# Kernel optimization log

Hardware: AMD Instinct MI355X
Metric: run time of the kernel (lower is better)

Reference implementation:

```python
import jax, jax.numpy as jnp
from jax import lax
import numpy as np

B, L, OBS_DIM, ACT_DIM = 4, 1024, 60, 2
D_MODEL, N_LAYERS, D_STATE, D_CONV, EXPAND = 256, 4, 16, 4, 2
D_INNER = EXPAND * D_MODEL
DT_RANK = (D_MODEL + 15) // 16  # mamba_ssm default: ceil(d_model/16)


def setup_inputs() -> dict:
    key = jax.random.key(0)
    ks = jax.random.split(key, 12)
    rn = lambda k, s, sc: jax.random.normal(k, s, jnp.float32) * sc
    return {
        "obs_seq": jax.random.normal(ks[0], (B, L, OBS_DIM), jnp.float32),
        "input_proj_w": rn(ks[1], (D_MODEL, OBS_DIM), OBS_DIM ** -0.5),
        "input_proj_b": jnp.zeros((D_MODEL,), jnp.float32),
        "norm_w": jnp.ones((N_LAYERS, D_MODEL), jnp.float32),
        "norm_b": jnp.zeros((N_LAYERS, D_MODEL), jnp.float32),
        "in_proj_w": rn(ks[2], (N_LAYERS, 2 * D_INNER, D_MODEL), D_MODEL ** -0.5),
        "conv_w": rn(ks[3], (N_LAYERS, D_INNER, D_CONV), D_CONV ** -0.5),
        "conv_b": jnp.zeros((N_LAYERS, D_INNER), jnp.float32),
        "x_proj_w": rn(ks[4], (N_LAYERS, DT_RANK + 2 * D_STATE, D_INNER), D_INNER ** -0.5),
        "dt_proj_w": rn(ks[5], (N_LAYERS, D_INNER, DT_RANK), DT_RANK ** -0.5),
        "dt_proj_b": jnp.full((N_LAYERS, D_INNER), float(np.log(np.expm1(0.01))), jnp.float32),
        "A_log": jnp.log(jnp.broadcast_to(jnp.arange(1, D_STATE + 1, dtype=jnp.float32), (N_LAYERS, D_INNER, D_STATE))),
        "D_skip": jnp.ones((N_LAYERS, D_INNER), jnp.float32),
        "out_proj_w": rn(ks[6], (N_LAYERS, D_MODEL, D_INNER), D_INNER ** -0.5),
        "policy_mean_w": rn(ks[7], (ACT_DIM, D_MODEL), 0.01 * D_MODEL ** -0.5),
        "policy_mean_b": jnp.zeros((ACT_DIM,), jnp.float32),
        "policy_log_std": jnp.zeros((ACT_DIM,), jnp.float32),
        "value_w": rn(ks[8], (1, D_MODEL), D_MODEL ** -0.5),
        "value_b": jnp.zeros((1,), jnp.float32),
    }


def _silu(x):
    return x * jax.nn.sigmoid(x)


def _layer_norm(x, w, b):
    m = jnp.mean(x, -1, keepdims=True)
    v = jnp.mean(jnp.square(x - m), -1, keepdims=True)
    return (x - m) * lax.rsqrt(v + 1e-5) * w + b


def _mamba(x, in_w, cw, cb, xw, dtw, dtb, a_log, d_skip, ow):
    # x: (B, L, d_model)
    xz = jnp.einsum('bld,ed->ble', x, in_w)            # (B, L, 2*d_inner)
    xi, z = xz[..., :D_INNER], xz[..., D_INNER:]
    # depthwise causal conv, width D_CONV
    xp = jnp.pad(xi, ((0, 0), (D_CONV - 1, 0), (0, 0)))
    conv = sum(xp[:, k:k + L, :] * cw[:, k] for k in range(D_CONV)) + cb
    xi = _silu(conv)
    dbc = jnp.einsum('bld,ed->ble', xi, xw)            # (B, L, dt_rank + 2*d_state)
    dt = jax.nn.softplus(jnp.einsum('blr,dr->bld', dbc[..., :DT_RANK], dtw) + dtb)
    Bm = dbc[..., DT_RANK:DT_RANK + D_STATE]           # (B, L, N)
    Cm = dbc[..., DT_RANK + D_STATE:]                  # (B, L, N)
    A = -jnp.exp(a_log)                                # (d_inner, N)
    dA = jnp.exp(dt[..., None] * A)                    # (B, L, d_inner, N)
    dBx = (dt * xi)[..., None] * Bm[:, :, None, :]     # (B, L, d_inner, N)

    def comb(c1, c2):
        a1, b1 = c1
        a2, b2 = c2
        return a2 * a1, a2 * b1 + b2

    _, h = lax.associative_scan(comb, (dA, dBx), axis=1)  # h_t = dA_t*h_{t-1} + dBx_t
    y = jnp.einsum('bldn,bln->bld', h, Cm) + d_skip * xi
    return jnp.einsum('bld,ed->ble', y * _silu(z), ow)


def _forward(obs_seq, input_proj_w, input_proj_b, norm_w, norm_b, in_proj_w, conv_w,
             conv_b, x_proj_w, dt_proj_w, dt_proj_b, A_log, D_skip, out_proj_w,
             policy_mean_w, policy_mean_b, policy_log_std, value_w, value_b):
    x = _silu(jnp.einsum('blo,do->bld', obs_seq, input_proj_w) + input_proj_b)
    for i in range(N_LAYERS):  # pre-norm residual Mamba blocks
        x = x + _mamba(_layer_norm(x, norm_w[i], norm_b[i]), in_proj_w[i], conv_w[i],
                       conv_b[i], x_proj_w[i], dt_proj_w[i], dt_proj_b[i], A_log[i],
                       D_skip[i], out_proj_w[i])
    mu = jnp.einsum('bld,ad->bla', x, policy_mean_w) + policy_mean_b
    std = jnp.broadcast_to(jnp.exp(policy_log_std), mu.shape)
    value = jnp.einsum('bld,od->blo', x, value_w) + value_b
    return mu, std, value


def reference(obs_seq, input_proj_w, input_proj_b, norm_w, norm_b, in_proj_w, conv_w,
              conv_b, x_proj_w, dt_proj_w, dt_proj_b, A_log, D_skip, out_proj_w,
              policy_mean_w, policy_mean_b, policy_log_std, value_w, value_b):
    return _forward(obs_seq, input_proj_w, input_proj_b, norm_w, norm_b, in_proj_w,
                    conv_w, conv_b, x_proj_w, dt_proj_w, dt_proj_b, A_log, D_skip,
                    out_proj_w, policy_mean_w, policy_mean_b, policy_log_std,
                    value_w, value_b)
```

## Files before the change

### kernel.cpp

```cpp
#include <hip/hip_runtime.h>
#include <hip/hip_bf16.h>

#define Bsz 4
#define Lseq 1024
#define OBS 60
#define DM 256
#define DI 512
#define DTR 16
#define DST 16
#define NTOK (Bsz*Lseq)
#define NCH 64
#define CH  16

typedef _Float16 half8 __attribute__((ext_vector_type(8)));
typedef float floatx4 __attribute__((ext_vector_type(4)));

__device__ __forceinline__ float silu_f(float v) {
    return v * (1.f / (1.f + __expf(-v)));
}
__device__ __forceinline__ float softplus_f(float v) {
    return fmaxf(v, 0.f) + log1pf(__expf(-fabsf(v)));
}

__device__ __forceinline__ void compute_dA(float dtv, const float* An,
                                           bool structured, float* dA) {
    if (structured) {
        float p1 = __expf(-dtv);
        float p2 = p1*p1, p4 = p2*p2, p8 = p4*p4;
        dA[0]=p1;      dA[1]=p2;      dA[2]=p2*p1;    dA[3]=p4;
        dA[4]=p4*p1;   dA[5]=p4*p2;   dA[6]=p4*dA[2]; dA[7]=p8;
        dA[8]=p8*p1;   dA[9]=p8*p2;   dA[10]=p8*dA[2];dA[11]=p8*p4;
        dA[12]=p8*dA[4];dA[13]=p8*dA[5];dA[14]=p8*dA[6];dA[15]=p8*p8;
    } else {
        #pragma unroll
        for (int n = 0; n < 16; ++n) dA[n] = __expf(dtv*An[n]);
    }
}

#define NIN_W  (4*1024*256)
#define NX_W   (4*64*512)
#define NOUT_W (4*256*512)
#define NCWT   (4*4*512)
#define NW_TOT (NIN_W + NX_W + NOUT_W + NCWT)
#define NWB    ((NW_TOT + 255)/256)
__global__ __launch_bounds__(256) void prep_kernel(
    const float* __restrict__ inw, const float* __restrict__ xw,
    const float* __restrict__ ow, const float* __restrict__ cw,
    _Float16* __restrict__ wh_in, _Float16* __restrict__ wh_x,
    _Float16* __restrict__ wh_out, _Float16* __restrict__ cwT,
    const float* __restrict__ obs, const float* __restrict__ ipw,
    const float* __restrict__ ipb, const float* __restrict__ nw,
    const float* __restrict__ nb, float* __restrict__ x,
    _Float16* __restrict__ xn_h) {
    __shared__ float so[OBS];
    __shared__ float ps[4];
    __shared__ float mean_s, rstd_s;
    int tid = threadIdx.x;
    if (blockIdx.x < NWB) {
        int idx = blockIdx.x*256 + tid;
        if (idx < NIN_W) {
            wh_in[idx] = (_Float16)inw[idx];
        } else if (idx < NIN_W + NX_W) {
            int r = idx - NIN_W;
            int layer = r >> 15;
            int rem = r & 32767;
            int n = rem >> 9, k = rem & 511;
            wh_x[r] = (_Float16)((n < 48) ? xw[((size_t)layer*48 + n)*512 + k] : 0.f);
        } else if (idx < NIN_W + NX_W + NOUT_W) {
            int r = idx - NIN_W - NX_W;
            wh_out[r] = (_Float16)ow[r];
        } else if (idx < NW_TOT) {
            int r = idx - NIN_W - NX_W - NOUT_W;
            int layer = r >> 11;
            int rem = r & 2047;
            int k = rem >> 9, d = rem & 511;
            cwT[r] = (_Float16)cw[layer*2048 + d*4 + k];
        }
        return;
    }
    int t = blockIdx.x - NWB;
    if (tid < OBS) so[tid] = obs[t*OBS + tid];
    __syncthreads();
    float acc = ipb[tid];
    const float* wr = ipw + tid*OBS;
    #pragma unroll
    for (int k = 0; k < OBS; ++k) acc += so[k]*wr[k];
    float v = silu_f(acc);
    x[t*DM + tid] = v;
    float s = v;
    #pragma unroll
    for (int off = 32; off; off >>= 1) s += __shfl_down(s, off);
    int wid = tid >> 6, lane = tid & 63;
    if (lane == 0) ps[wid] = s;
    __syncthreads();
    if (tid == 0) mean_s = (ps[0]+ps[1]+ps[2]+ps[3]) * (1.f/DM);
    __syncthreads();
    float m = mean_s;
    float d = v - m;
    float sq = d*d;
    #pragma unroll
    for (int off = 32; off; off >>= 1) sq += __shfl_down(sq, off);
    if (lane == 0) ps[wid] = sq;
    __syncthreads();
    if (tid == 0) rstd_s = rsqrtf((ps[0]+ps[1]+ps[2]+ps[3])*(1.f/DM) + 1e-5f);
    __syncthreads();
    xn_h[t*DM + tid] = (_Float16)(d * rstd_s * nw[tid] + nb[tid]);
}

template<int BM, int BN, int WM, int WN, int EPI>
__global__ __launch_bounds__(256) void hgemm_nt(
    const _Float16* __restrict__ A, const _Float16* __restrict__ W,
    void* __restrict__ Cout, const float* __restrict__ resid,
    int M, int N, int K, int ldc,
    const float* __restrict__ e0, const float* __restrict__ e1,
    const float* __restrict__ e2, const float* __restrict__ e3,
    const float* __restrict__ e4,
    float* __restrict__ xout, _Float16* __restrict__ xnh) {
    constexpr int MFR = BM/(WM*16);
    constexpr int NFR = BN/(WN*16);
    __shared__ _Float16 As[BM*64];
    __shared__ _Float16 Bs[BN*64];
    int tid = threadIdx.x;
    int r0 = blockIdx.y*BM, c0 = blockIdx.x*BN;
    int w = tid >> 6, lane = tid & 63;
    int wr = w / WN, wc = w % WN;
    floatx4 acc[MFR][NFR];
    #pragma unroll
    for (int i = 0; i < MFR; ++i)
        #pragma unroll
        for (int j = 0; j < NFR; ++j)
            acc[i][j] = (floatx4)0.f;

    for (int k0 = 0; k0 < K; k0 += 64) {
        #pragma unroll
        for (int c = 0; c < BM/32; ++c) {
            int q = tid + 256*c;
            int row = q >> 3, cc = (q & 7)*8;
            half8 v = *(const half8*)&A[(size_t)(r0 + row)*K + k0 + cc];
            *(half8*)&As[row*64 + (cc ^ ((row & 7) << 3))] = v;
        }
        #pragma unroll
        for (int c = 0; c < BN/32; ++c) {
            int q = tid + 256*c;
            int row = q >> 3, cc = (q & 7)*8;
            half8 v = *(const half8*)&W[(size_t)(c0 + row)*K + k0 + cc];
            *(half8*)&Bs[row*64 + (cc ^ ((row & 7) << 3))] = v;
        }
        __syncthreads();
        #pragma unroll
        for (int kc = 0; kc < 2; ++kc) {
            half8 a[MFR], b[NFR];
            int col = kc*32 + (lane >> 4)*8;
            #pragma unroll
            for (int i = 0; i < MFR; ++i) {
                int row = wr*(BM/WM) + i*16 + (lane & 15);
                a[i] = *(const half8*)&As[row*64 + (col ^ ((row & 7) << 3))];
            }
            #pragma unroll
            for (int j = 0; j < NFR; ++j) {
                int row = wc*(BN/WN) + j*16 + (lane & 15);
                b[j] = *(const half8*)&Bs[row*64 + (col ^ ((row & 7) << 3))];
            }
            #pragma unroll
            for (int i = 0; i < MFR; ++i)
                #pragma unroll
                for (int j = 0; j < NFR; ++j)
                    acc[i][j] = __builtin_amdgcn_mfma_f32_16x16x32_f16(a[i], b[j], acc[i][j], 0, 0, 0);
        }
        __syncthreads();
    }
    if constexpr (EPI == 1) {
        _Float16* C = (_Float16*)Cout;
        #pragma unroll
        for (int i = 0; i < MFR; ++i) {
            int m0 = r0 + wr*(BM/WM) + i*16 + (lane >> 4)*4;
            #pragma unroll
            for (int j = 0; j < NFR; ++j) {
                int col = c0 + wc*(BN/WN) + j*16 + (lane & 15);
                #pragma unroll
                for (int t = 0; t < 4; ++t)
                    C[(size_t)(m0 + t)*ldc + col] = (_Float16)acc[i][j][t];
            }
        }
    } else if constexpr (EPI == 2 || EPI == 3) {
        int g = lane >> 4, ln16 = lane & 15;
        #pragma unroll
        for (int t = 0; t < 4; ++t) {
            int row = r0 + wr*16 + g*4 + t;
            #pragma unroll
            for (int j = 0; j < NFR; ++j)
                acc[0][j][t] += resid[(size_t)row*DM + j*16 + ln16];
        }
        if constexpr (EPI == 2) {
            #pragma unroll
            for (int t = 0; t < 4; ++t) {
                int row = r0 + wr*16 + g*4 + t;
                float s = 0.f, sq = 0.f;
                #pragma unroll
                for (int j = 0; j < NFR; ++j) {
                    float v = acc[0][j][t];
                    xout[(size_t)row*DM + j*16 + ln16] = v;
                    s += v; sq += v*v;
                }
                #pragma unroll
                for (int msk = 1; msk < 16; msk <<= 1) {
                    s += __shfl_xor(s, msk);
                    sq += __shfl_xor(sq, msk);
                }
                float mean = s * (1.f/DM);
                float rstd = rsqrtf(sq*(1.f/DM) - mean*mean + 1e-5f);
                #pragma unroll
                for (int j = 0; j < NFR; ++j) {
                    int col = j*16 + ln16;
                    float v = acc[0][j][t];
                    xnh[(size_t)row*DM + col] =
                        (_Float16)((v - mean)*rstd*e0[col] + e1[col]);
                }
            }
        } else {
            float* out = xout;
            #pragma unroll
            for (int t = 0; t < 4; ++t) {
                int row = r0 + wr*16 + g*4 + t;
                float m0 = 0.f, m1 = 0.f, vv = 0.f;
                #pragma unroll
                for (int j = 0; j < NFR; ++j) {
                    int col = j*16 + ln16;
                    float v = acc[0][j][t];
                    m0 += v*e0[col]; m1 += v*e0[DM + col]; vv += v*e3[col];
                }
                #pragma unroll
                for (int msk = 1; msk < 16; msk <<= 1) {
                    m0 += __shfl_xor(m0, msk);
                    m1 += __shfl_xor(m1, msk);
                    vv += __shfl_xor(vv, msk);
                }
                if (ln16 == 0) {
                    out[row*2 + 0] = m0 + e1[0];
                    out[row*2 + 1] = m1 + e1[1];
                    out[2*NTOK + row*2 + 0] = __expf(e2[0]);
                    out[2*NTOK + row*2 + 1] = __expf(e2[1]);
                    out[4*NTOK + row] = vv + e4[0];
                }
            }
        }
    }
}

__global__ __launch_bounds__(256) void xproj_conv_gemm(
    const _Float16* __restrict__ xz_h, const _Float16* __restrict__ Wx,
    const _Float16* __restrict__ cwT, const float* __restrict__ cb,
    float* __restrict__ dbc) {
    __shared__ _Float16 As[32*64];
    __shared__ _Float16 Bs[64*64];
    int tid = threadIdx.x;
    int r0 = blockIdx.x*32;
    int w = tid >> 6, lane = tid & 63;
    int wr = w >> 1, wc = w & 1;
    floatx4 acc[2];
    acc[0] = (floatx4)0.f; acc[1] = (floatx4)0.f;
    for (int k0 = 0; k0 < 512; k0 += 64) {
        {
            int row = tid >> 3, e8 = tid & 7;
            int d = k0 + e8*8;
            int t = r0 + row, l = t & (Lseq-1);
            half8 zero8 = (half8)((_Float16)0.f);
            half8 v0 = (l >= 3) ? *(const half8*)&xz_h[(size_t)(t-3)*1024 + d] : zero8;
            half8 v1 = (l >= 2) ? *(const half8*)&xz_h[(size_t)(t-2)*1024 + d] : zero8;
            half8 v2 = (l >= 1) ? *(const half8*)&xz_h[(size_t)(t-1)*1024 + d] : zero8;
            half8 v3 = *(const half8*)&xz_h[(size_t)t*1024 + d];
            half8 c0 = *(const half8*)&cwT[0*512 + d];
            half8 c1 = *(const half8*)&cwT[1*512 + d];
            half8 c2 = *(const half8*)&cwT[2*512 + d];
            half8 c3 = *(const half8*)&cwT[3*512 + d];
            half8 o;
            #pragma unroll
            for (int e = 0; e < 8; ++e) {
                float a = cb[d + e];
                a += (float)v0[e]*(float)c0[e];
                a += (float)v1[e]*(float)c1[e];
                a += (float)v2[e]*(float)c2[e];
                a += (float)v3[e]*(float)c3[e];
                o[e] = (_Float16)silu_f(a);
            }
            *(half8*)&As[row*64 + ((e8*8) ^ ((row & 7) << 3))] = o;
        }
        #pragma unroll
        for (int c = 0; c < 2; ++c) {
            int q = tid + 256*c;
            int row = q >> 3, cc = (q & 7)*8;
            half8 vv = *(const half8*)&Wx[(size_t)row*512 + k0 + cc];
            *(half8*)&Bs[row*64 + (cc ^ ((row & 7) << 3))] = vv;
        }
        __syncthreads();
        #pragma unroll
        for (int kc = 0; kc < 2; ++kc) {
            int col = kc*32 + (lane >> 4)*8;
            int arow = wr*16 + (lane & 15);
            half8 a = *(const half8*)&As[arow*64 + (col ^ ((arow & 7) << 3))];
            #pragma unroll
            for (int j = 0; j < 2; ++j) {
                int brow = wc*32 + j*16 + (lane & 15);
                half8 b = *(const half8*)&Bs[brow*64 + (col ^ ((brow & 7) << 3))];
                acc[j] = __builtin_amdgcn_mfma_f32_16x16x32_f16(a, b, acc[j], 0, 0, 0);
            }
        }
        __syncthreads();
    }
    int m0 = r0 + wr*16 + (lane >> 4)*4;
    #pragma unroll
    for (int j = 0; j < 2; ++j) {
        int col = wc*32 + j*16 + (lane & 15);
        if (col < 48) {
            #pragma unroll
            for (int t = 0; t < 4; ++t)
                dbc[(size_t)(m0 + t)*48 + col] = acc[j][t];
        }
    }
}

__global__ __launch_bounds__(256) void scan_phaseA(
    const _Float16* __restrict__ xz_h, const float* __restrict__ dbc,
    const float* __restrict__ dtw, const float* __restrict__ dtb,
    const float* __restrict__ a_log, const float* __restrict__ cw,
    const float* __restrict__ cb,
    _Float16* __restrict__ xi_h,
    _Float16* __restrict__ Ap, _Float16* __restrict__ He) {
    __shared__ float sdbc[CH*48];
    int blk = blockIdx.x;
    int b = blk >> 7; int rem = blk & 127; int c = rem >> 1; int half = rem & 1;
    int d = half*256 + threadIdx.x;
    const float* src = dbc + ((size_t)(b*Lseq + c*CH))*48;
    for (int q = threadIdx.x; q < CH*48; q += 256) sdbc[q] = src[q];
    float wreg[16];
    #pragma unroll
    for (int r = 0; r < DTR; ++r) wreg[r] = dtw[d*DTR + r];
    float bias = dtb[d];
    float4 cwv = *(const float4*)&cw[d*4];
    float cbv = cb[d];
    float An[16];
    bool structured = true;
    #pragma unroll
    for (int n = 0; n < 16; ++n) {
        An[n] = -__expf(a_log[d*16 + n]);
        structured = structured && (fabsf(An[n] + (float)(n+1)) < 1e-4f*(n+1));
    }
    int l0 = c*CH; int t0 = b*Lseq + l0;
    float w0 = 0.f, w1 = 0.f, w2 = 0.f;
    if (l0 >= 3) {
        w0 = (float)xz_h[(size_t)(t0-3)*1024 + d];
        w1 = (float)xz_h[(size_t)(t0-2)*1024 + d];
        w2 = (float)xz_h[(size_t)(t0-1)*1024 + d];
    }
    __syncthreads();
    float h[16] = {};
    float ap[16];
    #pragma unroll
    for (int n = 0; n < 16; ++n) ap[n] = 1.f;
    for (int s = 0; s < CH; ++s) {
        float cur = (float)xz_h[(size_t)(t0+s)*1024 + d];
        float conv = cbv + cwv.x*w0 + cwv.y*w1 + cwv.z*w2 + cwv.w*cur;
        w0 = w1; w1 = w2; w2 = cur;
        float xiv = silu_f(conv);
        float dl = bias;
        #pragma unroll
        for (int r = 0; r < DTR; ++r) dl += sdbc[s*48 + r]*wreg[r];
        float dtv = softplus_f(dl);
        xi_h[(size_t)(t0+s)*DI + d] = (_Float16)xiv;
        float u = dtv*xiv;
        float dA[16];
        compute_dA(dtv, An, structured, dA);
        #pragma unroll
        for (int n = 0; n < 16; ++n) {
            h[n] = dA[n]*h[n] + u*sdbc[s*48 + DTR + n];
            ap[n] *= dA[n];
        }
    }
    size_t base = ((size_t)(b*NCH + c)*16)*DI + d;
    #pragma unroll
    for (int n = 0; n < 16; ++n) {
        Ap[base + n*DI] = (_Float16)ap[n];
        He[base + n*DI] = (_Float16)h[n];
    }
}

__global__ __launch_bounds__(256) void scan_phaseB(
    const _Float16* __restrict__ Ap, const _Float16* __restrict__ He,
    _Float16* __restrict__ h0) {
    int g = blockIdx.x*blockDim.x + threadIdx.x;
    int b = g >> 13; int n = (g >> 9) & 15; int d = g & 511;
    float run = 0.f;
    for (int c = 0; c < NCH; ++c) {
        size_t idx = ((size_t)(b*NCH + c)*16 + n)*DI + d;
        float a = (float)Ap[idx], e = (float)He[idx];
        h0[idx] = (_Float16)run;
        run = a*run + e;
    }
}

__global__ __launch_bounds__(256) void scan_phaseC(
    const _Float16* __restrict__ xi_h, const float* __restrict__ dbc,
    const float* __restrict__ dtw, const float* __restrict__ dtb,
    const float* __restrict__ a_log, const float* __restrict__ dskip,
    const _Float16* __restrict__ xz_h, const _Float16* __restrict__ h0,
    _Float16* __restrict__ yg_h) {
    __shared__ float sdbc[CH*48];
    int blk = blockIdx.x;
    int b = blk >> 7; int rem = blk & 127; int c = rem >> 1; int half = rem & 1;
    int d = half*256 + threadIdx.x;
    const float* src = dbc + ((size_t)(b*Lseq + c*CH))*48;
    for (int q = threadIdx.x; q < CH*48; q += 256) sdbc[q] = src[q];
    float wreg[16];
    #pragma unroll
    for (int r = 0; r < DTR; ++r) wreg[r] = dtw[d*DTR + r];
    float bias = dtb[d];
    float An[16];
    bool structured = true;
    #pragma unroll
    for (int n = 0; n < 16; ++n) {
        An[n] = -__expf(a_log[d*16 + n]);
        structured = structured && (fabsf(An[n] + (float)(n+1)) < 1e-4f*(n+1));
    }
    __syncthreads();
    int t0 = b*Lseq + c*CH;
    float h[16];
    size_t base = ((size_t)(b*NCH + c)*16)*DI + d;
    #pragma unroll
    for (int n = 0; n < 16; ++n) h[n] = (float)h0[base + n*DI];
    float ds = dskip[d];
    for (int s = 0; s < CH; ++s) {
        size_t ti = (size_t)(t0+s)*DI + d;
        float xiv = (float)xi_h[ti];
        float dl = bias;
        #pragma unroll
        for (int r = 0; r < DTR; ++r) dl += sdbc[s*48 + r]*wreg[r];
        float dtv = softplus_f(dl);
        float u = dtv*xiv;
        float dA[16];
        compute_dA(dtv, An, structured, dA);
        float y = ds*xiv;
        #pragma unroll
        for (int n = 0; n < 16; ++n) {
            h[n] = dA[n]*h[n] + u*sdbc[s*48 + DTR + n];
            y += h[n]*sdbc[s*48 + DTR + DST + n];
        }
        float zv = (float)xz_h[(size_t)(t0+s)*1024 + DI + d];
        yg_h[ti] = (_Float16)(y * silu_f(zv));
    }
}

extern "C" void kernel_launch(void* const* d_in, const int* in_sizes, int n_in,
                              void* d_out, int out_size, void* d_ws, size_t ws_size,
                              hipStream_t stream) {
    const float* obs = (const float*)d_in[0];
    const float* ipw = (const float*)d_in[1];
    const float* ipb = (const float*)d_in[2];
    const float* nw  = (const float*)d_in[3];
    const float* nb  = (const float*)d_in[4];
    const float* inw = (const float*)d_in[5];
    const float* cw  = (const float*)d_in[6];
    const float* cb  = (const float*)d_in[7];
    const float* xw  = (const float*)d_in[8];
    const float* dtw = (const float*)d_in[9];
    const float* dtb = (const float*)d_in[10];
    const float* alog= (const float*)d_in[11];
    const float* dsk = (const float*)d_in[12];
    const float* ow  = (const float*)d_in[13];
    const float* pw  = (const float*)d_in[14];
    const float* pb  = (const float*)d_in[15];
    const float* ls  = (const float*)d_in[16];
    const float* vw  = (const float*)d_in[17];
    const float* vb  = (const float*)d_in[18];
    float* out = (float*)d_out;

    float* ws = (float*)d_ws;
    float* x   = ws;
    float* dbc = x   + 1048576;
    _Float16* f16b  = (_Float16*)(dbc + 196608);
    _Float16* xz_h  = f16b;
    _Float16* xn_h  = xz_h  + 4194304;
    _Float16* xi_h  = xn_h  + 1048576;
    _Float16* yg_h  = xi_h  + 2097152;
    _Float16* Ap_h  = yg_h  + 2097152;
    _Float16* He_h  = Ap_h  + 2097152;
    _Float16* h0_h  = Ap_h;
    _Float16* wh_in = He_h  + 2097152;
    _Float16* wh_x  = wh_in + 1048576;
    _Float16* wh_out= wh_x  + 131072;
    _Float16* cwT_h = wh_out+ 524288;

    prep_kernel<<<NWB + NTOK, 256, 0, stream>>>(
        inw, xw, ow, cw, wh_in, wh_x, wh_out, cwT_h,
        obs, ipw, ipb, nw, nb, x, xn_h);

    for (int i = 0; i < 4; ++i) {
        {
            dim3 g(1024/64, NTOK/128);
            hgemm_nt<128,64,2,2,1><<<g, 256, 0, stream>>>(
                xn_h, wh_in + (size_t)i*1024*256, xz_h, nullptr, NTOK, 1024, 256, 1024,
                nullptr, nullptr, nullptr, nullptr, nullptr, nullptr, nullptr);
        }
        xproj_conv_gemm<<<NTOK/32, 256, 0, stream>>>(
            xz_h, wh_x + (size_t)i*64*512, cwT_h + i*2048, cb + i*DI, dbc);
        scan_phaseA<<<Bsz*NCH*2, 256, 0, stream>>>(
            xz_h, dbc, dtw + (size_t)i*DI*DTR, dtb + i*DI,
            alog + (size_t)i*DI*DST, cw + (size_t)i*DI*4, cb + i*DI,
            xi_h, Ap_h, He_h);
        scan_phaseB<<<128, 256, 0, stream>>>(Ap_h, He_h, h0_h);
        scan_phaseC<<<Bsz*NCH*2, 256, 0, stream>>>(
            xi_h, dbc, dtw + (size_t)i*DI*DTR, dtb + i*DI,
            alog + (size_t)i*DI*DST, dsk + i*DI, xz_h, h0_h, yg_h);
        {
            dim3 g(1, NTOK/64);
            if (i < 3) {
                hgemm_nt<64,256,4,1,2><<<g, 256, 0, stream>>>(
                    yg_h, wh_out + (size_t)i*256*512, nullptr, x, NTOK, 256, 512, 256,
                    nw + (i+1)*DM, nb + (i+1)*DM, nullptr, nullptr, nullptr, x, xn_h);
            } else {
                hgemm_nt<64,256,4,1,3><<<g, 256, 0, stream>>>(
                    yg_h, wh_out + (size_t)i*256*512, nullptr, x, NTOK, 256, 512, 256,
                    pw, pb, ls, vw, vb, out, nullptr);
            }
        }
    }
}
```

Measured before the change: 346.0 us.

## Fold dt_proj into x_proj weights and precompute dt via one fused GEMM

Precomputes the product of dt_proj and the dt rows of x_proj in the prep kernel, so a single GEMM (576 columns) produces the softplus'd dt per channel plus the B/C projections. The causal conv and SiLU move into a separate elementwise kernel that writes xi once. The scan kernels then read precomputed dt and xi from memory instead of recomputing the 16-term dt dot product and the conv per step, and they prefetch per-chunk inputs into registers. The cost is a much larger GEMM (512 extra output columns), an extra kernel launch, and an extra fp16 dt buffer written and read in every layer.

```diff
diff --git a/kernel.cpp b/kernel.cpp
--- a/kernel.cpp
+++ b/kernel.cpp
@@ -38,47 +38,68 @@
 }
 
 #define NIN_W  (4*1024*256)
-#define NX_W   (4*64*512)
 #define NOUT_W (4*256*512)
-#define NCWT   (4*4*512)
-#define NW_TOT (NIN_W + NX_W + NOUT_W + NCWT)
-#define NWB    ((NW_TOT + 255)/256)
+#define NS0    (NIN_W + NOUT_W)
+#define NB_S0  (NS0/256)
+#define NB_S1  (4*64*512/256)
+#define NB_S2  32
 __global__ __launch_bounds__(256) void prep_kernel(
-    const float* __restrict__ inw, const float* __restrict__ xw,
-    const float* __restrict__ ow, const float* __restrict__ cw,
-    _Float16* __restrict__ wh_in, _Float16* __restrict__ wh_x,
-    _Float16* __restrict__ wh_out, _Float16* __restrict__ cwT,
+    const float* __restrict__ inw, const float* __restrict__ ow,
+    const float* __restrict__ xw, const float* __restrict__ dtw,
+    _Float16* __restrict__ wh_in, _Float16* __restrict__ wh_out,
+    _Float16* __restrict__ Wbig,
     const float* __restrict__ obs, const float* __restrict__ ipw,
     const float* __restrict__ ipb, const float* __restrict__ nw,
     const float* __restrict__ nb, float* __restrict__ x,
     _Float16* __restrict__ xn_h) {
-    __shared__ float so[OBS];
+    __shared__ float swxT[512][16];
     __shared__ float ps[4];
     __shared__ float mean_s, rstd_s;
     int tid = threadIdx.x;
-    if (blockIdx.x < NWB) {
+    if (blockIdx.x < NB_S0) {
         int idx = blockIdx.x*256 + tid;
-        if (idx < NIN_W) {
-            wh_in[idx] = (_Float16)inw[idx];
-        } else if (idx < NIN_W + NX_W) {
-            int r = idx - NIN_W;
-            int layer = r >> 15;
-            int rem = r & 32767;
-            int n = rem >> 9, k = rem & 511;
-            wh_x[r] = (_Float16)((n < 48) ? xw[((size_t)layer*48 + n)*512 + k] : 0.f);
-        } else if (idx < NIN_W + NX_W + NOUT_W) {
-            int r = idx - NIN_W - NX_W;
-            wh_out[r] = (_Float16)ow[r];
-        } else if (idx < NW_TOT) {
-            int r = idx - NIN_W - NX_W - NOUT_W;
-            int layer = r >> 11;
-            int rem = r & 2047;
-            int k = rem >> 9, d = rem & 511;
-            cwT[r] = (_Float16)cw[layer*2048 + d*4 + k];
-        }
+        if (idx < NIN_W) wh_in[idx] = (_Float16)inw[idx];
+        else wh_out[idx - NIN_W] = (_Float16)ow[idx - NIN_W];
         return;
     }
-    int t = blockIdx.x - NWB;
+    if (blockIdx.x < NB_S0 + NB_S1) {
+        int idx = (blockIdx.x - NB_S0)*256 + tid;
+        int L = idx >> 15;
+        int rem = idx & 32767;
+        int j = rem >> 9, k = rem & 511;
+        float v = (j < 32) ? xw[(size_t)L*48*512 + (size_t)(16 + j)*512 + k] : 0.f;
+        Wbig[(size_t)L*576*512 + (size_t)(512 + j)*512 + k] = (_Float16)v;
+        return;
+    }
+    if (blockIdx.x < NB_S0 + NB_S1 + NB_S2) {
+        int q2 = blockIdx.x - NB_S0 - NB_S1;
+        int L = q2 >> 3, E = q2 & 7;
+        const float* xwL = xw + (size_t)L*48*512;
+        #pragma unroll
+        for (int i = 0; i < 32; ++i) {
+            int q = tid + 256*i;
+            int r = q >> 9, k = q & 511;
+            swxT[k][r] = xwL[(size_t)r*512 + k];
+        }
+        __syncthreads();
+        int e = E*64 + (tid >> 2), kq = tid & 3;
+        float dwr[16];
+        const float* dtwp = dtw + ((size_t)L*512 + e)*16;
+        #pragma unroll
+        for (int r = 0; r < 16; ++r) dwr[r] = dtwp[r];
+        _Float16* wb = Wbig + (size_t)L*576*512 + (size_t)e*512;
+        for (int kk = 0; kk < 128; ++kk) {
+            int k = kq*128 + kk;
+            const float* sp = &swxT[k][0];
+            float acc = 0.f;
+            #pragma unroll
+            for (int r = 0; r < 16; ++r) acc += dwr[r]*sp[r];
+            wb[k] = (_Float16)acc;
+        }
+        return;
+    }
+    int t = blockIdx.x - NB_S0 - NB_S1 - NB_S2;
+    __shared__ float so[OBS];
     if (tid < OBS) so[tid] = obs[t*OBS + tid];
     __syncthreads();
     float acc = ipb[tid];
@@ -96,15 +117,15 @@
     if (tid == 0) mean_s = (ps[0]+ps[1]+ps[2]+ps[3]) * (1.f/DM);
     __syncthreads();
     float m = mean_s;
-    float d = v - m;
-    float sq = d*d;
+    float dd = v - m;
+    float sq = dd*dd;
     #pragma unroll
     for (int off = 32; off; off >>= 1) sq += __shfl_down(sq, off);
     if (lane == 0) ps[wid] = sq;
     __syncthreads();
     if (tid == 0) rstd_s = rsqrtf((ps[0]+ps[1]+ps[2]+ps[3])*(1.f/DM) + 1e-5f);
     __syncthreads();
-    xn_h[t*DM + tid] = (_Float16)(d * rstd_s * nw[tid] + nb[tid]);
+    xn_h[t*DM + tid] = (_Float16)(dd * rstd_s * nw[tid] + nb[tid]);
 }
 
 template<int BM, int BN, int WM, int WN, int EPI>
@@ -247,50 +268,46 @@
     }
 }
 
-__global__ __launch_bounds__(256) void xproj_conv_gemm(
-    const _Float16* __restrict__ xz_h, const _Float16* __restrict__ Wx,
-    const _Float16* __restrict__ cwT, const float* __restrict__ cb,
-    float* __restrict__ dbc) {
+__global__ __launch_bounds__(256) void conv_silu_kernel(
+    const _Float16* __restrict__ xz_h, const float* __restrict__ cw,
+    const float* __restrict__ cb, _Float16* __restrict__ xi_h) {
+    int idx = blockIdx.x*blockDim.x + threadIdx.x;
+    if (idx >= NTOK*DI) return;
+    int d = idx & (DI-1); int t = idx >> 9;
+    int l = t & (Lseq-1);
+    float acc = cb[d];
+    #pragma unroll
+    for (int k = 0; k < 4; ++k) {
+        int ls = l - 3 + k;
+        if (ls >= 0) acc += (float)xz_h[(size_t)(t-3+k)*1024 + d] * cw[d*4 + k];
+    }
+    xi_h[idx] = (_Float16)silu_f(acc);
+}
+
+__global__ __launch_bounds__(256) void big_gemm(
+    const _Float16* __restrict__ xi_h, const _Float16* __restrict__ Wb,
+    const float* __restrict__ dtb, _Float16* __restrict__ dt_h,
+    float* __restrict__ dbc32) {
     __shared__ _Float16 As[32*64];
     __shared__ _Float16 Bs[64*64];
     int tid = threadIdx.x;
-    int r0 = blockIdx.x*32;
+    int r0 = blockIdx.y*32, c0 = blockIdx.x*64;
     int w = tid >> 6, lane = tid & 63;
     int wr = w >> 1, wc = w & 1;
     floatx4 acc[2];
     acc[0] = (floatx4)0.f; acc[1] = (floatx4)0.f;
     for (int k0 = 0; k0 < 512; k0 += 64) {
         {
-            int row = tid >> 3, e8 = tid & 7;
-            int d = k0 + e8*8;
-            int t = r0 + row, l = t & (Lseq-1);
-            half8 zero8 = (half8)((_Float16)0.f);
-            half8 v0 = (l >= 3) ? *(const half8*)&xz_h[(size_t)(t-3)*1024 + d] : zero8;
-            half8 v1 = (l >= 2) ? *(const half8*)&xz_h[(size_t)(t-2)*1024 + d] : zero8;
-            half8 v2 = (l >= 1) ? *(const half8*)&xz_h[(size_t)(t-1)*1024 + d] : zero8;
-            half8 v3 = *(const half8*)&xz_h[(size_t)t*1024 + d];
-            half8 c0 = *(const half8*)&cwT[0*512 + d];
-            half8 c1 = *(const half8*)&cwT[1*512 + d];
-            half8 c2 = *(const half8*)&cwT[2*512 + d];
-            half8 c3 = *(const half8*)&cwT[3*512 + d];
-            half8 o;
-            #pragma unroll
-            for (int e = 0; e < 8; ++e) {
-                float a = cb[d + e];
-                a += (float)v0[e]*(float)c0[e];
-                a += (float)v1[e]*(float)c1[e];
-                a += (float)v2[e]*(float)c2[e];
-                a += (float)v3[e]*(float)c3[e];
-                o[e] = (_Float16)silu_f(a);
-            }
-            *(half8*)&As[row*64 + ((e8*8) ^ ((row & 7) << 3))] = o;
+            int row = tid >> 3, cc = (tid & 7)*8;
+            half8 v = *(const half8*)&xi_h[(size_t)(r0 + row)*512 + k0 + cc];
+            *(half8*)&As[row*64 + (cc ^ ((row & 7) << 3))] = v;
         }
         #pragma unroll
         for (int c = 0; c < 2; ++c) {
             int q = tid + 256*c;
             int row = q >> 3, cc = (q & 7)*8;
-            half8 vv = *(const half8*)&Wx[(size_t)row*512 + k0 + cc];
-            *(half8*)&Bs[row*64 + (cc ^ ((row & 7) << 3))] = vv;
+            half8 v = *(const half8*)&Wb[(size_t)(c0 + row)*512 + k0 + cc];
+            *(half8*)&Bs[row*64 + (cc ^ ((row & 7) << 3))] = v;
         }
         __syncthreads();
         #pragma unroll
@@ -308,36 +325,38 @@
         __syncthreads();
     }
     int m0 = r0 + wr*16 + (lane >> 4)*4;
+    int bx = blockIdx.x;
     #pragma unroll
     for (int j = 0; j < 2; ++j) {
-        int col = wc*32 + j*16 + (lane & 15);
-        if (col < 48) {
+        int lc = wc*32 + j*16 + (lane & 15);
+        if (bx < 8) {
+            int col = c0 + lc;
+            float bias = dtb[col];
             #pragma unroll
             for (int t = 0; t < 4; ++t)
-                dbc[(size_t)(m0 + t)*48 + col] = acc[j][t];
+                dt_h[(size_t)(m0 + t)*512 + col] = (_Float16)softplus_f(acc[j][t] + bias);
+        } else if (lc < 32) {
+            #pragma unroll
+            for (int t = 0; t < 4; ++t)
+                dbc32[(size_t)(m0 + t)*32 + lc] = acc[j][t];
         }
     }
 }
 
 __global__ __launch_bounds__(256) void scan_phaseA(
-    const _Float16* __restrict__ xz_h, const float* __restrict__ dbc,
-    const float* __restrict__ dtw, const float* __restrict__ dtb,
-    const float* __restrict__ a_log, const float* __restrict__ cw,
-    const float* __restrict__ cb,
-    _Float16* __restrict__ xi_h,
+    const _Float16* __restrict__ xi_h, const _Float16* __restrict__ dt_h,
+    const float* __restrict__ dbc32, const float* __restrict__ a_log,
     _Float16* __restrict__ Ap, _Float16* __restrict__ He) {
-    __shared__ float sdbc[CH*48];
+    __shared__ __align__(16) float sdbc[CH*32];
     int blk = blockIdx.x;
     int b = blk >> 7; int rem = blk & 127; int c = rem >> 1; int half = rem & 1;
     int d = half*256 + threadIdx.x;
-    const float* src = dbc + ((size_t)(b*Lseq + c*CH))*48;
-    for (int q = threadIdx.x; q < CH*48; q += 256) sdbc[q] = src[q];
-    float wreg[16];
-    #pragma unroll
-    for (int r = 0; r < DTR; ++r) wreg[r] = dtw[d*DTR + r];
-    float bias = dtb[d];
-    float4 cwv = *(const float4*)&cw[d*4];
-    float cbv = cb[d];
+    {
+        const float* src = dbc32 + ((size_t)(b*Lseq + c*CH))*32;
+        int q = threadIdx.x;
+        sdbc[q] = src[q];
+        sdbc[q + 256] = src[q + 256];
+    }
     float An[16];
     bool structured = true;
     #pragma unroll
@@ -345,34 +364,31 @@
         An[n] = -__expf(a_log[d*16 + n]);
         structured = structured && (fabsf(An[n] + (float)(n+1)) < 1e-4f*(n+1));
     }
-    int l0 = c*CH; int t0 = b*Lseq + l0;
-    float w0 = 0.f, w1 = 0.f, w2 = 0.f;
-    if (l0 >= 3) {
-        w0 = (float)xz_h[(size_t)(t0-3)*1024 + d];
-        w1 = (float)xz_h[(size_t)(t0-2)*1024 + d];
-        w2 = (float)xz_h[(size_t)(t0-1)*1024 + d];
+    int t0 = b*Lseq + c*CH;
+    float xiv[CH], dtv[CH];
+    #pragma unroll
+    for (int s = 0; s < CH; ++s) {
+        xiv[s] = (float)xi_h[(size_t)(t0+s)*DI + d];
+        dtv[s] = (float)dt_h[(size_t)(t0+s)*DI + d];
     }
     __syncthreads();
     float h[16] = {};
     float ap[16];
     #pragma unroll
     for (int n = 0; n < 16; ++n) ap[n] = 1.f;
+    #pragma unroll
     for (int s = 0; s < CH; ++s) {
-        float cur = (float)xz_h[(size_t)(t0+s)*1024 + d];
-        float conv = cbv + cwv.x*w0 + cwv.y*w1 + cwv.z*w2 + cwv.w*cur;
-        w0 = w1; w1 = w2; w2 = cur;
-        float xiv = silu_f(conv);
-        float dl = bias;
-        #pragma unroll
-        for (int r = 0; r < DTR; ++r) dl += sdbc[s*48 + r]*wreg[r];
-        float dtv = softplus_f(dl);
-        xi_h[(size_t)(t0+s)*DI + d] = (_Float16)xiv;
-        float u = dtv*xiv;
+        float u = dtv[s]*xiv[s];
         float dA[16];
-        compute_dA(dtv, An, structured, dA);
+        compute_dA(dtv[s], An, structured, dA);
+        float Bv[16];
+        *(float4*)&Bv[0]  = *(const float4*)&sdbc[s*32 + 0];
+        *(float4*)&Bv[4]  = *(const float4*)&sdbc[s*32 + 4];
+        *(float4*)&Bv[8]  = *(const float4*)&sdbc[s*32 + 8];
+        *(float4*)&Bv[12] = *(const float4*)&sdbc[s*32 + 12];
         #pragma unroll
         for (int n = 0; n < 16; ++n) {
-            h[n] = dA[n]*h[n] + u*sdbc[s*48 + DTR + n];
+            h[n] = dA[n]*h[n] + u*Bv[n];
             ap[n] *= dA[n];
         }
     }
@@ -399,21 +415,20 @@
 }
 
 __global__ __launch_bounds__(256) void scan_phaseC(
-    const _Float16* __restrict__ xi_h, const float* __restrict__ dbc,
-    const float* __restrict__ dtw, const float* __restrict__ dtb,
-    const float* __restrict__ a_log, const float* __restrict__ dskip,
-    const _Float16* __restrict__ xz_h, const _Float16* __restrict__ h0,
-    _Float16* __restrict__ yg_h) {
-    __shared__ float sdbc[CH*48];
+    const _Float16* __restrict__ xi_h, const _Float16* __restrict__ dt_h,
+    const float* __restrict__ dbc32, const float* __restrict__ a_log,
+    const float* __restrict__ dskip, const _Float16* __restrict__ xz_h,
+    const _Float16* __restrict__ h0, _Float16* __restrict__ yg_h) {
+    __shared__ __align__(16) float sdbc[CH*32];
     int blk = blockIdx.x;
     int b = blk >> 7; int rem = blk & 127; int c = rem >> 1; int half = rem & 1;
     int d = half*256 + threadIdx.x;
-    const float* src = dbc + ((size_t)(b*Lseq + c*CH))*48;
-    for (int q = threadIdx.x; q < CH*48; q += 256) sdbc[q] = src[q];
-    float wreg[16];
-    #pragma unroll
-    for (int r = 0; r < DTR; ++r) wreg[r] = dtw[d*DTR + r];
-    float bias = dtb[d];
+    {
+        const float* src = dbc32 + ((size_t)(b*Lseq + c*CH))*32;
+        int q = threadIdx.x;
+        sdbc[q] = src[q];
+        sdbc[q + 256] = src[q + 256];
+    }
     float An[16];
     bool structured = true;
     #pragma unroll
@@ -421,31 +436,41 @@
         An[n] = -__expf(a_log[d*16 + n]);
         structured = structured && (fabsf(An[n] + (float)(n+1)) < 1e-4f*(n+1));
     }
-    __syncthreads();
     int t0 = b*Lseq + c*CH;
+    float xiv[CH], dtv[CH], zv[CH];
+    #pragma unroll
+    for (int s = 0; s < CH; ++s) {
+        xiv[s] = (float)xi_h[(size_t)(t0+s)*DI + d];
+        dtv[s] = (float)dt_h[(size_t)(t0+s)*DI + d];
+        zv[s]  = (float)xz_h[(size_t)(t0+s)*1024 + DI + d];
+    }
+    __syncthreads();
     float h[16];
     size_t base = ((size_t)(b*NCH + c)*16)*DI + d;
     #pragma unroll
     for (int n = 0; n < 16; ++n) h[n] = (float)h0[base + n*DI];
     float ds = dskip[d];
+    #pragma unroll
     for (int s = 0; s < CH; ++s) {
-        size_t ti = (size_t)(t0+s)*DI + d;
-        float xiv = (float)xi_h[ti];
-        float dl = bias;
-        #pragma unroll
-        for (int r = 0; r < DTR; ++r) dl += sdbc[s*48 + r]*wreg[r];
-        float dtv = softplus_f(dl);
-        float u = dtv*xiv;
+        float u = dtv[s]*xiv[s];
         float dA[16];
-        compute_dA(dtv, An, structured, dA);
-        float y = ds*xiv;
+        compute_dA(dtv[s], An, structured, dA);
+        float Bv[16], Cv[16];
+        *(float4*)&Bv[0]  = *(const float4*)&sdbc[s*32 + 0];
+        *(float4*)&Bv[4]  = *(const float4*)&sdbc[s*32 + 4];
+        *(float4*)&Bv[8]  = *(const float4*)&sdbc[s*32 + 8];
+        *(float4*)&Bv[12] = *(const float4*)&sdbc[s*32 + 12];
+        *(float4*)&Cv[0]  = *(const float4*)&sdbc[s*32 + 16];
+        *(float4*)&Cv[4]  = *(const float4*)&sdbc[s*32 + 20];
+        *(float4*)&Cv[8]  = *(const float4*)&sdbc[s*32 + 24];
+        *(float4*)&Cv[12] = *(const float4*)&sdbc[s*32 + 28];
+        float y = ds*xiv[s];
         #pragma unroll
         for (int n = 0; n < 16; ++n) {
-            h[n] = dA[n]*h[n] + u*sdbc[s*48 + DTR + n];
-            y += h[n]*sdbc[s*48 + DTR + DST + n];
-        }
-        float zv = (float)xz_h[(size_t)(t0+s)*1024 + DI + d];
-        yg_h[ti] = (_Float16)(y * silu_f(zv));
+            h[n] = dA[n]*h[n] + u*Bv[n];
+            y += h[n]*Cv[n];
+        }
+        yg_h[(size_t)(t0+s)*DI + d] = (_Float16)(y * silu_f(zv[s]));
     }
 }
 
@@ -474,23 +499,23 @@
     float* out = (float*)d_out;
 
     float* ws = (float*)d_ws;
-    float* x   = ws;
-    float* dbc = x   + 1048576;
-    _Float16* f16b  = (_Float16*)(dbc + 196608);
+    float* x     = ws;
+    float* dbc32 = x + 1048576;
+    _Float16* f16b  = (_Float16*)(dbc32 + 131072);
     _Float16* xz_h  = f16b;
     _Float16* xn_h  = xz_h  + 4194304;
     _Float16* xi_h  = xn_h  + 1048576;
-    _Float16* yg_h  = xi_h  + 2097152;
+    _Float16* dt_h  = xi_h  + 2097152;
+    _Float16* yg_h  = dt_h  + 2097152;
     _Float16* Ap_h  = yg_h  + 2097152;
     _Float16* He_h  = Ap_h  + 2097152;
     _Float16* h0_h  = Ap_h;
     _Float16* wh_in = He_h  + 2097152;
-    _Float16* wh_x  = wh_in + 1048576;
-    _Float16* wh_out= wh_x  + 131072;
-    _Float16* cwT_h = wh_out+ 524288;
-
-    prep_kernel<<<NWB + NTOK, 256, 0, stream>>>(
-        inw, xw, ow, cw, wh_in, wh_x, wh_out, cwT_h,
+    _Float16* wh_out= wh_in + 1048576;
+    _Float16* Wbig  = wh_out+ 524288;
+
+    prep_kernel<<<NB_S0 + NB_S1 + NB_S2 + NTOK, 256, 0, stream>>>(
+        inw, ow, xw, dtw, wh_in, wh_out, Wbig,
         obs, ipw, ipb, nw, nb, x, xn_h);
 
     for (int i = 0; i < 4; ++i) {
@@ -500,16 +525,19 @@
                 xn_h, wh_in + (size_t)i*1024*256, xz_h, nullptr, NTOK, 1024, 256, 1024,
                 nullptr, nullptr, nullptr, nullptr, nullptr, nullptr, nullptr);
         }
-        xproj_conv_gemm<<<NTOK/32, 256, 0, stream>>>(
-            xz_h, wh_x + (size_t)i*64*512, cwT_h + i*2048, cb + i*DI, dbc);
+        conv_silu_kernel<<<(NTOK*DI)/256, 256, 0, stream>>>(
+            xz_h, cw + (size_t)i*DI*4, cb + i*DI, xi_h);
+        {
+            dim3 g(9, NTOK/32);
+            big_gemm<<<g, 256, 0, stream>>>(
+                xi_h, Wbig + (size_t)i*576*512, dtb + i*DI, dt_h, dbc32);
+        }
         scan_phaseA<<<Bsz*NCH*2, 256, 0, stream>>>(
-            xz_h, dbc, dtw + (size_t)i*DI*DTR, dtb + i*DI,
-            alog + (size_t)i*DI*DST, cw + (size_t)i*DI*4, cb + i*DI,
-            xi_h, Ap_h, He_h);
+            xi_h, dt_h, dbc32, alog + (size_t)i*DI*DST, Ap_h, He_h);
         scan_phaseB<<<128, 256, 0, stream>>>(Ap_h, He_h, h0_h);
         scan_phaseC<<<Bsz*NCH*2, 256, 0, stream>>>(
-            xi_h, dbc, dtw + (size_t)i*DI*DTR, dtb + i*DI,
-            alog + (size_t)i*DI*DST, dsk + i*DI, xz_h, h0_h, yg_h);
+            xi_h, dt_h, dbc32, alog + (size_t)i*DI*DST,
+            dsk + i*DI, xz_h, h0_h, yg_h);
         {
             dim3 g(1, NTOK/64);
             if (i < 3) {
```

Measured after the change: 371.7 us. 1.07x slower.

## Cache dt in phase A, use chunk-major layout and vectorized scan loads

Applied to the files above, without the earlier changes.

Phase A now also stores the softplus dt values alongside xi in a per-thread chunk-contiguous layout, so phase C reads them back instead of recomputing the dt projection. Ap/He/h0 switch to the same [chunk][d][n] layout with half8 vector stores and loads, and phase B indexing is adjusted to match. Global loads of xz are hoisted ahead of the barrier and shared-memory B/C/dt reads become float4 loads. In exchange, an extra dt buffer is written and read, register pressure rises from the unrolled arrays, and the strided per-thread 32-byte accesses may coalesce worse than the previous d-contiguous layout.

```diff
diff --git a/kernel.cpp b/kernel.cpp
--- a/kernel.cpp
+++ b/kernel.cpp
@@ -324,9 +324,9 @@
     const float* __restrict__ dtw, const float* __restrict__ dtb,
     const float* __restrict__ a_log, const float* __restrict__ cw,
     const float* __restrict__ cb,
-    _Float16* __restrict__ xi_h,
+    _Float16* __restrict__ xi_c, _Float16* __restrict__ dt_c,
     _Float16* __restrict__ Ap, _Float16* __restrict__ He) {
-    __shared__ float sdbc[CH*48];
+    __shared__ __align__(16) float sdbc[CH*48];
     int blk = blockIdx.x;
     int b = blk >> 7; int rem = blk & 127; int c = rem >> 1; int half = rem & 1;
     int d = half*256 + threadIdx.x;
@@ -352,46 +352,72 @@
         w1 = (float)xz_h[(size_t)(t0-2)*1024 + d];
         w2 = (float)xz_h[(size_t)(t0-1)*1024 + d];
     }
+    float cur[CH];
+    #pragma unroll
+    for (int s = 0; s < CH; ++s)
+        cur[s] = (float)xz_h[(size_t)(t0+s)*1024 + d];
     __syncthreads();
     float h[16] = {};
     float ap[16];
     #pragma unroll
     for (int n = 0; n < 16; ++n) ap[n] = 1.f;
+    half8 xlv[2], dlv[2];
+    #pragma unroll
     for (int s = 0; s < CH; ++s) {
-        float cur = (float)xz_h[(size_t)(t0+s)*1024 + d];
-        float conv = cbv + cwv.x*w0 + cwv.y*w1 + cwv.z*w2 + cwv.w*cur;
-        w0 = w1; w1 = w2; w2 = cur;
+        float conv = cbv + cwv.x*w0 + cwv.y*w1 + cwv.z*w2 + cwv.w*cur[s];
+        w0 = w1; w1 = w2; w2 = cur[s];
         float xiv = silu_f(conv);
-        float dl = bias;
-        #pragma unroll
-        for (int r = 0; r < DTR; ++r) dl += sdbc[s*48 + r]*wreg[r];
-        float dtv = softplus_f(dl);
-        xi_h[(size_t)(t0+s)*DI + d] = (_Float16)xiv;
+        float4 q0 = *(const float4*)&sdbc[s*48 + 0];
+        float4 q1 = *(const float4*)&sdbc[s*48 + 4];
+        float4 q2 = *(const float4*)&sdbc[s*48 + 8];
+        float4 q3 = *(const float4*)&sdbc[s*48 + 12];
+        float dlin = bias
+            + q0.x*wreg[0] + q0.y*wreg[1] + q0.z*wreg[2] + q0.w*wreg[3]
+            + q1.x*wreg[4] + q1.y*wreg[5] + q1.z*wreg[6] + q1.w*wreg[7]
+            + q2.x*wreg[8] + q2.y*wreg[9] + q2.z*wreg[10] + q2.w*wreg[11]
+            + q3.x*wreg[12] + q3.y*wreg[13] + q3.z*wreg[14] + q3.w*wreg[15];
+        float dtv = softplus_f(dlin);
+        xlv[s >> 3][s & 7] = (_Float16)xiv;
+        dlv[s >> 3][s & 7] = (_Float16)dtv;
         float u = dtv*xiv;
         float dA[16];
         compute_dA(dtv, An, structured, dA);
+        float Bv[16];
+        *(float4*)&Bv[0]  = *(const float4*)&sdbc[s*48 + 16];
+        *(float4*)&Bv[4]  = *(const float4*)&sdbc[s*48 + 20];
+        *(float4*)&Bv[8]  = *(const float4*)&sdbc[s*48 + 24];
+        *(float4*)&Bv[12] = *(const float4*)&sdbc[s*48 + 28];
         #pragma unroll
         for (int n = 0; n < 16; ++n) {
-            h[n] = dA[n]*h[n] + u*sdbc[s*48 + DTR + n];
+            h[n] = dA[n]*h[n] + u*Bv[n];
             ap[n] *= dA[n];
         }
     }
-    size_t base = ((size_t)(b*NCH + c)*16)*DI + d;
+    size_t cbase = ((size_t)(b*NCH + c)*DI + d)*16;
+    *(half8*)&xi_c[cbase + 0] = xlv[0];
+    *(half8*)&xi_c[cbase + 8] = xlv[1];
+    *(half8*)&dt_c[cbase + 0] = dlv[0];
+    *(half8*)&dt_c[cbase + 8] = dlv[1];
+    half8 apv[2], hev[2];
     #pragma unroll
     for (int n = 0; n < 16; ++n) {
-        Ap[base + n*DI] = (_Float16)ap[n];
-        He[base + n*DI] = (_Float16)h[n];
-    }
+        apv[n >> 3][n & 7] = (_Float16)ap[n];
+        hev[n >> 3][n & 7] = (_Float16)h[n];
+    }
+    *(half8*)&Ap[cbase + 0] = apv[0];
+    *(half8*)&Ap[cbase + 8] = apv[1];
+    *(half8*)&He[cbase + 0] = hev[0];
+    *(half8*)&He[cbase + 8] = hev[1];
 }
 
 __global__ __launch_bounds__(256) void scan_phaseB(
     const _Float16* __restrict__ Ap, const _Float16* __restrict__ He,
     _Float16* __restrict__ h0) {
     int g = blockIdx.x*blockDim.x + threadIdx.x;
-    int b = g >> 13; int n = (g >> 9) & 15; int d = g & 511;
+    int b = g >> 13; int dn = g & 8191;
     float run = 0.f;
     for (int c = 0; c < NCH; ++c) {
-        size_t idx = ((size_t)(b*NCH + c)*16 + n)*DI + d;
+        size_t idx = ((size_t)(b*NCH + c)*DI)*16 + dn;
         float a = (float)Ap[idx], e = (float)He[idx];
         h0[idx] = (_Float16)run;
         run = a*run + e;
@@ -399,21 +425,16 @@
 }
 
 __global__ __launch_bounds__(256) void scan_phaseC(
-    const _Float16* __restrict__ xi_h, const float* __restrict__ dbc,
-    const float* __restrict__ dtw, const float* __restrict__ dtb,
-    const float* __restrict__ a_log, const float* __restrict__ dskip,
-    const _Float16* __restrict__ xz_h, const _Float16* __restrict__ h0,
-    _Float16* __restrict__ yg_h) {
-    __shared__ float sdbc[CH*48];
+    const _Float16* __restrict__ xi_c, const _Float16* __restrict__ dt_c,
+    const float* __restrict__ dbc, const float* __restrict__ a_log,
+    const float* __restrict__ dskip, const _Float16* __restrict__ xz_h,
+    const _Float16* __restrict__ h0, _Float16* __restrict__ yg_h) {
+    __shared__ __align__(16) float sdbc[CH*48];
     int blk = blockIdx.x;
     int b = blk >> 7; int rem = blk & 127; int c = rem >> 1; int half = rem & 1;
     int d = half*256 + threadIdx.x;
     const float* src = dbc + ((size_t)(b*Lseq + c*CH))*48;
     for (int q = threadIdx.x; q < CH*48; q += 256) sdbc[q] = src[q];
-    float wreg[16];
-    #pragma unroll
-    for (int r = 0; r < DTR; ++r) wreg[r] = dtw[d*DTR + r];
-    float bias = dtb[d];
     float An[16];
     bool structured = true;
     #pragma unroll
@@ -421,31 +442,47 @@
         An[n] = -__expf(a_log[d*16 + n]);
         structured = structured && (fabsf(An[n] + (float)(n+1)) < 1e-4f*(n+1));
     }
-    __syncthreads();
     int t0 = b*Lseq + c*CH;
+    size_t cbase = ((size_t)(b*NCH + c)*DI + d)*16;
+    half8 xlv[2], dlv[2], h0v[2];
+    xlv[0] = *(const half8*)&xi_c[cbase + 0];
+    xlv[1] = *(const half8*)&xi_c[cbase + 8];
+    dlv[0] = *(const half8*)&dt_c[cbase + 0];
+    dlv[1] = *(const half8*)&dt_c[cbase + 8];
+    h0v[0] = *(const half8*)&h0[cbase + 0];
+    h0v[1] = *(const half8*)&h0[cbase + 8];
+    float zv[CH];
+    #pragma unroll
+    for (int s = 0; s < CH; ++s)
+        zv[s] = (float)xz_h[(size_t)(t0+s)*1024 + DI + d];
+    __syncthreads();
     float h[16];
-    size_t base = ((size_t)(b*NCH + c)*16)*DI + d;
-    #pragma unroll
-    for (int n = 0; n < 16; ++n) h[n] = (float)h0[base + n*DI];
+    #pragma unroll
+    for (int n = 0; n < 16; ++n) h[n] = (float)h0v[n >> 3][n & 7];
     float ds = dskip[d];
+    #pragma unroll
     for (int s = 0; s < CH; ++s) {
-        size_t ti = (size_t)(t0+s)*DI + d;
-        float xiv = (float)xi_h[ti];
-        float dl = bias;
-        #pragma unroll
-        for (int r = 0; r < DTR; ++r) dl += sdbc[s*48 + r]*wreg[r];
-        float dtv = softplus_f(dl);
+        float xiv = (float)xlv[s >> 3][s & 7];
+        float dtv = (float)dlv[s >> 3][s & 7];
         float u = dtv*xiv;
         float dA[16];
         compute_dA(dtv, An, structured, dA);
+        float Bv[16], Cv[16];
+        *(float4*)&Bv[0]  = *(const float4*)&sdbc[s*48 + 16];
+        *(float4*)&Bv[4]  = *(const float4*)&sdbc[s*48 + 20];
+        *(float4*)&Bv[8]  = *(const float4*)&sdbc[s*48 + 24];
+        *(float4*)&Bv[12] = *(const float4*)&sdbc[s*48 + 28];
+        *(float4*)&Cv[0]  = *(const float4*)&sdbc[s*48 + 32];
+        *(float4*)&Cv[4]  = *(const float4*)&sdbc[s*48 + 36];
+        *(float4*)&Cv[8]  = *(const float4*)&sdbc[s*48 + 40];
+        *(float4*)&Cv[12] = *(const float4*)&sdbc[s*48 + 44];
         float y = ds*xiv;
         #pragma unroll
         for (int n = 0; n < 16; ++n) {
-            h[n] = dA[n]*h[n] + u*sdbc[s*48 + DTR + n];
-            y += h[n]*sdbc[s*48 + DTR + DST + n];
-        }
-        float zv = (float)xz_h[(size_t)(t0+s)*1024 + DI + d];
-        yg_h[ti] = (_Float16)(y * silu_f(zv));
+            h[n] = dA[n]*h[n] + u*Bv[n];
+            y += h[n]*Cv[n];
+        }
+        yg_h[(size_t)(t0+s)*DI + d] = (_Float16)(y * silu_f(zv[s]));
     }
 }
 
@@ -479,8 +516,9 @@
     _Float16* f16b  = (_Float16*)(dbc + 196608);
     _Float16* xz_h  = f16b;
     _Float16* xn_h  = xz_h  + 4194304;
-    _Float16* xi_h  = xn_h  + 1048576;
-    _Float16* yg_h  = xi_h  + 2097152;
+    _Float16* xi_c  = xn_h  + 1048576;
+    _Float16* dt_c  = xi_c  + 2097152;
+    _Float16* yg_h  = dt_c  + 2097152;
     _Float16* Ap_h  = yg_h  + 2097152;
     _Float16* He_h  = Ap_h  + 2097152;
     _Float16* h0_h  = Ap_h;
@@ -505,11 +543,11 @@
         scan_phaseA<<<Bsz*NCH*2, 256, 0, stream>>>(
             xz_h, dbc, dtw + (size_t)i*DI*DTR, dtb + i*DI,
             alog + (size_t)i*DI*DST, cw + (size_t)i*DI*4, cb + i*DI,
-            xi_h, Ap_h, He_h);
+            xi_c, dt_c, Ap_h, He_h);
         scan_phaseB<<<128, 256, 0, stream>>>(Ap_h, He_h, h0_h);
         scan_phaseC<<<Bsz*NCH*2, 256, 0, stream>>>(
-            xi_h, dbc, dtw + (size_t)i*DI*DTR, dtb + i*DI,
-            alog + (size_t)i*DI*DST, dsk + i*DI, xz_h, h0_h, yg_h);
+            xi_c, dt_c, dbc, alog + (size_t)i*DI*DST,
+            dsk + i*DI, xz_h, h0_h, yg_h);
         {
             dim3 g(1, NTOK/64);
             if (i < 3) {
```

Result: slower. 374.9 us (+8.4%).
